# Kernel optimization log

Hardware: AMD Instinct MI355X
Metric: run time of the kernel (lower is better)

## Reference

```python
import jax, jax.numpy as jnp
import numpy as np

N, E, G = 50000, 800000, 128
IN, HID, OUT, H = 38, 64, 128, 4
NEG_SLOPE = 0.2
EPS = 1e-16


def setup_inputs() -> dict:
    key = jax.random.key(0)
    ks = jax.random.split(key, 16)
    s = 0.05
    inp = {
        "x": jax.random.normal(ks[0], (N, IN), jnp.float32),
        "edge_index": jax.random.randint(ks[1], (2, E), 0, N),
        "batch": jnp.sort(jax.random.randint(ks[2], (N,), 0, G)),
        # GATv2 layer 1: in=38 -> heads=4, C=64 (concat -> 256)
        "Wl1": jax.random.normal(ks[3], (IN, H * HID), jnp.float32) * s,
        "bl1": jnp.zeros((H * HID,), jnp.float32),
        "Wr1": jax.random.normal(ks[4], (IN, H * HID), jnp.float32) * s,
        "br1": jnp.zeros((H * HID,), jnp.float32),
        "att1": jax.random.normal(ks[5], (H, HID), jnp.float32) * s,
        "bias1": jnp.zeros((H * HID,), jnp.float32),
        # GATv2 layer 2: in=256 -> heads=1, C=128
        "Wl2": jax.random.normal(ks[6], (H * HID, OUT), jnp.float32) * s,
        "bl2": jnp.zeros((OUT,), jnp.float32),
        "Wr2": jax.random.normal(ks[7], (H * HID, OUT), jnp.float32) * s,
        "br2": jnp.zeros((OUT,), jnp.float32),
        "att2": jax.random.normal(ks[8], (1, OUT), jnp.float32) * s,
        "bias2": jnp.zeros((OUT,), jnp.float32),
    }
    return inp


def gatv2(x, src, dst, Wl, bl, Wr, br, att, bias, heads, C):
    n = x.shape[0]
    xl = (x @ Wl + bl).reshape(n, heads, C)  # source transform
    xr = (x @ Wr + br).reshape(n, heads, C)  # target transform
    e = jax.nn.leaky_relu(xl[src] + xr[dst], NEG_SLOPE)  # [E', H, C]
    logits = jnp.einsum("ehc,hc->eh", e, att)
    # segment softmax over incoming edges of each destination node
    m = jax.ops.segment_max(logits, dst, num_segments=n)
    p = jnp.exp(logits - m[dst])
    denom = jax.ops.segment_sum(p, dst, num_segments=n)
    alpha = p / (denom[dst] + EPS)  # [E', H]
    msg = xl[src] * alpha[..., None]
    out = jax.ops.segment_sum(msg, dst, num_segments=n)  # [N, H, C]
    return out.reshape(n, heads * C) + bias


def reference(x, edge_index, batch, Wl1, bl1, Wr1, br1, att1, bias1,
              Wl2, bl2, Wr2, br2, att2, bias2):
    n = x.shape[0]
    loops = jnp.arange(n, dtype=edge_index.dtype)
    src = jnp.concatenate([edge_index[0], loops])  # add_self_loops (PyG default)
    dst = jnp.concatenate([edge_index[1], loops])
    h = jax.nn.relu(gatv2(x, src, dst, Wl1, bl1, Wr1, br1, att1, bias1, H, HID))
    # dropout is identity at inference
    h = jax.nn.relu(gatv2(h, src, dst, Wl2, bl2, Wr2, br2, att2, bias2, 1, OUT))
    # global mean pool over graphs
    sums = jax.ops.segment_sum(h, batch, num_segments=G)
    counts = jax.ops.segment_sum(jnp.ones((n,), h.dtype), batch, num_segments=G)
    return sums / jnp.maximum(counts, 1.0)[:, None]
```

## Files before the change

### kernel.cpp

```cpp
#include <hip/hip_runtime.h>
#include <hip/hip_bf16.h>
#include <limits.h>

#define N_NODES 50000
#define N_EDGES 800000
#define TOT_E   (N_EDGES + N_NODES)
#define IN_F    38
#define HIDC    64
#define NH      4
#define F1      256
#define F2      128
#define NGRAPH  128
#define NEG_SLOPE 0.2f
#define EPS_A   1e-16f

typedef __hip_bfloat16 bf16;
typedef unsigned char fp8_t;
typedef __attribute__((ext_vector_type(8))) short short8;
typedef __attribute__((ext_vector_type(16))) float f32x16;
typedef __attribute__((ext_vector_type(2))) float f2;

constexpr size_t al256(size_t x) { return (x + 255) & ~(size_t)255; }

#define P_WL1   0
#define P_BL1   (P_WL1 + IN_F * F1)
#define P_WR1   (P_BL1 + F1)
#define P_BR1   (P_WR1 + IN_F * F1)
#define P_ATT1  (P_BR1 + F1)
#define P_BIAS1 (P_ATT1 + F1)
#define P_WL2   (P_BIAS1 + F1)
#define P_BL2   (P_WL2 + F1 * F2)
#define P_WR2   (P_BL2 + F2)
#define P_BR2   (P_WR2 + F1 * F2)
#define P_ATT2  (P_BR2 + F2)
#define P_BIAS2 (P_ATT2 + F2)
#define P_TOTAL (P_BIAS2 + F2)

constexpr size_t OFF_PAR  = 256;
constexpr size_t OFF_XL1  = OFF_PAR + al256((size_t)P_TOTAL * 4);
constexpr size_t OFF_XR1  = OFF_XL1 + al256((size_t)N_NODES * F1 * 2);
constexpr size_t OFF_H    = OFF_XR1 + al256((size_t)N_NODES * F1 * 2);
constexpr size_t OFF_XL2  = OFF_H   + al256((size_t)N_NODES * F1 * 2);
constexpr size_t OFF_XR2  = OFF_XL2 + al256((size_t)N_NODES * F2 * 2);
constexpr size_t OFF_CNT  = OFF_XR2 + al256((size_t)N_NODES * F2 * 2);
constexpr size_t OFF_GS   = OFF_CNT + al256((size_t)N_NODES * 4);
constexpr size_t OFF_GE   = OFF_GS  + al256((size_t)NGRAPH * 4);
constexpr size_t OFF_PSUM = OFF_GE  + al256((size_t)NGRAPH * 4);
constexpr size_t OFF_ZEND = OFF_PSUM+ al256((size_t)NGRAPH * F2 * 4);
constexpr size_t OFF_OFFS = OFF_ZEND;
constexpr size_t OFF_CSR  = OFF_OFFS+ al256((size_t)(N_NODES + 1) * 4);
constexpr size_t OFF_WT1  = OFF_CSR + al256((size_t)TOT_E * 4);
constexpr size_t OFF_WT2  = OFF_WT1 + al256((size_t)512 * 64 * 2);
constexpr size_t OFF_BS   = OFF_WT2 + al256((size_t)256 * 256 * 2);
constexpr size_t OFF_RANK = OFF_BS  + al256(64 * 4);
constexpr size_t OFF_H2   = OFF_XL1;
constexpr size_t OFF_XB   = OFF_H;

#define SCAN_BLKS 49
#define GBLK 1563
#define SBL  831

__device__ __forceinline__ void unpack8bf2(uint4 q, f2* f) {
  unsigned v[4] = {q.x, q.y, q.z, q.w};
#pragma unroll
  for (int i = 0; i < 4; i++) {
    f2 t;
    t.x = __uint_as_float(v[i] << 16);
    t.y = __uint_as_float(v[i] & 0xffff0000u);
    f[i] = t;
  }
}

__device__ __forceinline__ void load8bf2(const bf16* __restrict__ p, f2* f) {
  unpack8bf2(*(const uint4*)p, f);
}

__device__ __forceinline__ void unpack8fp8(uint2 q, f2* f) {
  f[0] = __builtin_amdgcn_cvt_pk_f32_fp8(q.x, false);
  f[1] = __builtin_amdgcn_cvt_pk_f32_fp8(q.x, true);
  f[2] = __builtin_amdgcn_cvt_pk_f32_fp8(q.y, false);
  f[3] = __builtin_amdgcn_cvt_pk_f32_fp8(q.y, true);
}

__device__ __forceinline__ fp8_t f32_to_fp8(float v) {
  return (fp8_t)(__builtin_amdgcn_cvt_pk_fp8_f32(v, v, 0, false) & 0xFF);
}

__device__ __forceinline__ f2 lrelu2(f2 s) {
  f2 as;
  as.x = __uint_as_float(__float_as_uint(s.x) & 0x7fffffffu);
  as.y = __uint_as_float(__float_as_uint(s.y) & 0x7fffffffu);
  return 0.6f * s + 0.4f * as;
}

__device__ __forceinline__ int detect_f32_wave(const void* __restrict__ x) {
  const unsigned short* u = (const unsigned short*)x;
  unsigned short b = u[threadIdx.x & 63];
  int e = (b >> 7) & 0xFF;
  unsigned long long m = __ballot(!((e == 0) || (e >= 96 && e <= 158)));
  return __popcll(m) > 8;
}

#define B_CVT  338
#define B_XP   1563
#define B_W1   128
#define B_W2   256
#define B_BND  196
#define B_CNT  831

struct PrepArgs {
  const void* x;
  const void* src[12];
  const int* ei;
  const int* batch;
};

__global__ __launch_bounds__(256) void prep_k(
    PrepArgs a, float* __restrict__ par, bf16* __restrict__ xb,
    bf16* __restrict__ wt1, bf16* __restrict__ wt2,
    int* __restrict__ gs, int* __restrict__ ge, int* __restrict__ cnt,
    int* __restrict__ rank) {
  int b = blockIdx.x;
  const int tid = threadIdx.x;

  if (b < B_CVT) {
    const int flag = detect_f32_wave(a.x);
    int idx = b * 256 + tid;
    const void* p; int base;
    if      (idx < P_BL1)  { p = a.src[0];  base = P_WL1; }
    else if (idx < P_WR1)  { p = a.src[1];  base = P_BL1; }
    else if (idx < P_BR1)  { p = a.src[2];  base = P_WR1; }
    else if (idx < P_ATT1) { p = a.src[3];  base = P_BR1; }
    else if (idx < P_BIAS1){ p = a.src[4];  base = P_ATT1; }
    else if (idx < P_WL2)  { p = a.src[5];  base = P_BIAS1; }
    else if (idx < P_BL2)  { p = a.src[6];  base = P_WL2; }
    else if (idx < P_WR2)  { p = a.src[7];  base = P_BL2; }
    else if (idx < P_BR2)  { p = a.src[8];  base = P_WR2; }
    else if (idx < P_ATT2) { p = a.src[9];  base = P_BR2; }
    else if (idx < P_BIAS2){ p = a.src[10]; base = P_ATT2; }
    else                   { p = a.src[11]; base = P_BIAS2; }
    int li = idx - base;
    par[idx] = flag ? ((const float*)p)[li] : (float)((const bf16*)p)[li];
    return;
  }
  b -= B_CVT;
  if (b < B_XP) {
    const int flag = detect_f32_wave(a.x);
    int gid = b * 256 + tid;
    int n = gid >> 3, k0 = (gid & 7) * 8;
    float v[8];
#pragma unroll
    for (int j = 0; j < 8; j++) {
      int k = k0 + j;
      v[j] = 0.f;
      if (k < IN_F) {
        int idx = n * IN_F + k;
        v[j] = flag ? ((const float*)a.x)[idx] : (float)((const bf16*)a.x)[idx];
      }
    }
    __align__(16) bf16 ob[8];
#pragma unroll
    for (int j = 0; j < 8; j++) ob[j] = (bf16)v[j];
    *(uint4*)(xb + (size_t)n * 64 + k0) = *(uint4*)ob;
    return;
  }
  b -= B_XP;
  if (b < B_W1) {
    const int flag = detect_f32_wave(a.x);
    int i = b * 256 + tid;
    int n = i >> 6, k = i & 63;
    float v = 0.f;
    if (k < IN_F) {
      const void* W = (n < F1) ? a.src[0] : a.src[2];
      int col = (n < F1) ? n : n - F1;
      int idx = k * F1 + col;
      v = flag ? ((const float*)W)[idx] : (float)((const bf16*)W)[idx];
    }
    wt1[i] = (bf16)v;
    return;
  }
  b -= B_W1;
  if (b < B_W2) {
    const int flag = detect_f32_wave(a.x);
    int i = b * 256 + tid;
    int n = i >> 8, k = i & 255;
    const void* W = (n < F2) ? a.src[6] : a.src[8];
    int col = (n < F2) ? n : n - F2;
    int idx = k * F2 + col;
    float v = flag ? ((const float*)W)[idx] : (float)((const bf16*)W)[idx];
    wt2[i] = (bf16)v;
    return;
  }
  b -= B_W2;
  if (b < B_BND) {
    int n = b * 256 + tid;
    if (n >= N_NODES) return;
    int bb = a.batch[n];
    if (n == 0) gs[bb] = 1;
    else {
      int bp = a.batch[n - 1];
      if (bp != bb) { gs[bb] = n + 1; ge[bp] = n; }
    }
    if (n == N_NODES - 1) ge[bb] = N_NODES;
    return;
  }
  b -= B_BND;
  {
    int base = b * 1024 + tid;
    int dstv[4]; bool val[4];
#pragma unroll
    for (int i = 0; i < 4; i++) {
      int e = base + i * 256;
      val[i] = e < TOT_E;
      dstv[i] = 0;
      if (val[i])
        dstv[i] = (e < N_EDGES) ? a.ei[N_EDGES + e] : (e - N_EDGES);
    }
#pragma unroll
    for (int i = 0; i < 4; i++) {
      int e = base + i * 256;
      if (val[i]) rank[e] = atomicAdd(&cnt[dstv[i]], 1);
    }
  }
}

__global__ __launch_bounds__(256) void gemm1_scatter_k(
    const bf16* __restrict__ xb, const bf16* __restrict__ wt1,
    const float* __restrict__ par,
    fp8_t* __restrict__ xl1, bf16* __restrict__ xr1,
    const int* __restrict__ ei, const int* __restrict__ offs,
    const int* __restrict__ rank, int* __restrict__ csr) {
  __shared__ char lds[24576];
  if (blockIdx.x >= GBLK) {
    int base = (blockIdx.x - GBLK) * 1024 + threadIdx.x;
#pragma unroll
    for (int i = 0; i < 4; i++) {
      int e = base + i * 256;
      if (e >= TOT_E) continue;
      int src, dst;
      if (e < N_EDGES) { src = ei[e]; dst = ei[N_EDGES + e]; }
      else             { src = dst = e - N_EDGES; }
      csr[offs[dst] + rank[e]] = src;
    }
    return;
  }
  const int w = threadIdx.x >> 6, lane = threadIdx.x & 63;
  const int m0 = blockIdx.x * 32;
  const int colbase = w * 128;
  const int lm = lane & 31;
  const int kh = lane >> 5;

  int arow = m0 + lm; if (arow >= N_NODES) arow = N_NODES - 1;
  short8 afr[4];
#pragma unroll
  for (int kk = 0; kk < 4; kk++)
    afr[kk] = *(const short8*)(xb + (size_t)arow * 64 + kk * 16 + kh * 8);

  f32x16 acc[4] = {};
#pragma unroll
  for (int t = 0; t < 4; t++) {
    int n = colbase + t * 32 + lm;
#pragma unroll
    for (int kk = 0; kk < 4; kk++) {
      short8 b = *(const short8*)(wt1 + (size_t)n * 64 + kk * 16 + kh * 8);
      acc[t] = __builtin_amdgcn_mfma_f32_32x32x16_bf16(afr[kk], b, acc[t], 0, 0, 0);
    }
  }

  char* lds8  = lds;
  bf16* lds16 = (bf16*)(lds + 8192);
  if (w < 2) {
#pragma unroll
    for (int t = 0; t < 4; t++) {
      int col = colbase + t * 32 + lm;
      float bv = par[P_BL1 + col];
#pragma unroll
      for (int reg = 0; reg < 16; reg++) {
        int rl = (reg & 3) + 8 * (reg >> 2) + 4 * kh;
        lds8[rl * 256 + col] = f32_to_fp8(acc[t][reg] + bv);
      }
    }
  } else {
#pragma unroll
    for (int t = 0; t < 4; t++) {
      int c = colbase - 256 + t * 32 + lm;
      float bv = par[P_BR1 + c];
#pragma unroll
      for (int reg = 0; reg < 16; reg++) {
        int rl = (reg & 3) + 8 * (reg >> 2) + 4 * kh;
        lds16[rl * 256 + c] = (bf16)(acc[t][reg] + bv);
      }
    }
  }
  __syncthreads();

  const int tid = threadIdx.x;
#pragma unroll
  for (int i = 0; i < 2; i++) {
    int idx = tid + i * 256;
    int row = idx >> 4, ck = (idx & 15) * 16;
    int grow = m0 + row;
    if (grow < N_NODES)
      *(uint4*)(xl1 + (size_t)grow * F1 + ck) = *(uint4*)(lds8 + row * 256 + ck);
  }
#pragma unroll
  for (int i = 0; i < 4; i++) {
    int idx = tid + i * 256;
    int row = idx >> 5, ck = (idx & 31) * 16;
    int grow = m0 + row;
    if (grow < N_NODES)
      *(uint4*)((char*)(xr1 + (size_t)grow * F1) + ck) =
          *(uint4*)((char*)(lds16 + row * 256) + ck);
  }
}

__global__ __launch_bounds__(256) void gemm2_mfma_k(
    const bf16* __restrict__ h, const bf16* __restrict__ wt2,
    const float* __restrict__ par,
    fp8_t* __restrict__ xl2, bf16* __restrict__ xr2) {
  __shared__ char lds[12288];
  const int w = threadIdx.x >> 6, lane = threadIdx.x & 63;
  const int m0 = blockIdx.x * 32;
  const int colbase = w * 64;
  const int lm = lane & 31;
  const int kh = lane >> 5;

  int arow = m0 + lm; if (arow >= N_NODES) arow = N_NODES - 1;
  const bf16* hrow = h + (size_t)arow * F1 + kh * 8;

  f32x16 acc[2] = {};
#pragma unroll
  for (int kk = 0; kk < 16; kk++) {
    short8 a = *(const short8*)(hrow + kk * 16);
#pragma unroll
    for (int t = 0; t < 2; t++) {
      int n = colbase + t * 32 + lm;
      short8 b = *(const short8*)(wt2 + (size_t)n * 256 + kk * 16 + kh * 8);
      acc[t] = __builtin_amdgcn_mfma_f32_32x32x16_bf16(a, b, acc[t], 0, 0, 0);
    }
  }

  char* lds8  = lds;
  bf16* lds16 = (bf16*)(lds + 4096);
  if (w < 2) {
#pragma unroll
    for (int t = 0; t < 2; t++) {
      int col = colbase + t * 32 + lm;
      float bv = par[P_BL2 + col];
#pragma unroll
      for (int reg = 0; reg < 16; reg++) {
        int rl = (reg & 3) + 8 * (reg >> 2) + 4 * kh;
        lds8[rl * 128 + col] = f32_to_fp8(acc[t][reg] + bv);
      }
    }
  } else {
#pragma unroll
    for (int t = 0; t < 2; t++) {
      int c = colbase - 128 + t * 32 + lm;
      float bv = par[P_BR2 + c];
#pragma unroll
      for (int reg = 0; reg < 16; reg++) {
        int rl = (reg & 3) + 8 * (reg >> 2) + 4 * kh;
        lds16[rl * 128 + c] = (bf16)(acc[t][reg] + bv);
      }
    }
  }
  __syncthreads();

  const int tid = threadIdx.x;
  {
    int row = tid >> 3, ck = (tid & 7) * 16;
    int grow = m0 + row;
    if (grow < N_NODES)
      *(uint4*)(xl2 + (size_t)grow * F2 + ck) = *(uint4*)(lds8 + row * 128 + ck);
  }
#pragma unroll
  for (int i = 0; i < 2; i++) {
    int idx = tid + i * 256;
    int row = idx >> 4, ck = (idx & 15) * 16;
    int grow = m0 + row;
    if (grow < N_NODES)
      *(uint4*)((char*)(xr2 + (size_t)grow * F2) + ck) =
          *(uint4*)((char*)(lds16 + row * 128) + ck);
  }
}

__global__ __launch_bounds__(1024) void scan_a(const int* __restrict__ cnt,
                                               int* __restrict__ offs,
                                               int* __restrict__ bsum) {
  __shared__ int wsum[16];
  const int t = threadIdx.x;
  const int lane = t & 63, w = t >> 6;
  int idx = blockIdx.x * 1024 + t;
  int v = (idx < N_NODES) ? cnt[idx] : 0;
  int s = v;
#pragma unroll
  for (int off = 1; off < 64; off <<= 1) {
    int u = __shfl_up(s, off, 64);
    if (lane >= off) s += u;
  }
  if (lane == 63) wsum[w] = s;
  __syncthreads();
  int prefix = 0;
  for (int i = 0; i < w; i++) prefix += wsum[i];
  if (idx < N_NODES) offs[idx] = prefix + s - v;
  if (t == 1023) bsum[blockIdx.x] = prefix + s;
}

__global__ void scan_c(const int* __restrict__ bsum, int* __restrict__ offs) {
  const int t = threadIdx.x;
  const int grp = blockIdx.x >> 2;
  __shared__ int sboff;
  if (t < 64) {
    int v = (t < SCAN_BLKS) ? bsum[t] : 0;
    int s = v;
#pragma unroll
    for (int off = 1; off < 64; off <<= 1) {
      int u = __shfl_up(s, off, 64);
      if (t >= off) s += u;
    }
    if (t == grp) sboff = s - v;
  }
  __syncthreads();
  int idx = blockIdx.x * 256 + t;
  if (idx < N_NODES) offs[idx] += sboff;
  if (blockIdx.x == 0 && t == 0) offs[N_NODES] = TOT_E;
}

__global__ __launch_bounds__(256, 4) void agg1_k(
    const fp8_t* __restrict__ xl1, const bf16* __restrict__ xr1,
    const float* __restrict__ par,
    const int* __restrict__ offs, const int* __restrict__ csr,
    bf16* __restrict__ hout) {
  const int dst = blockIdx.x * 4 + (threadIdx.x >> 6);
  if (dst >= N_NODES) return;
  const int lane = threadIdx.x & 63;
  const int g = lane >> 5;
  const int sl = lane & 31;
  const int chb = sl * 8;

  f2 r2[4], a2[4];
  load8bf2(xr1 + (size_t)dst * F1 + chb, r2);
  {
    float4 aa = *(const float4*)(par + P_ATT1 + chb);
    float4 ab = *(const float4*)(par + P_ATT1 + chb + 4);
    a2[0].x = aa.x; a2[0].y = aa.y; a2[1].x = aa.z; a2[1].y = aa.w;
    a2[2].x = ab.x; a2[2].y = ab.y; a2[3].x = ab.z; a2[3].y = ab.w;
  }

  const int e0 = offs[dst], e1 = offs[dst + 1];
  const f2 zf2 = {0.f, 0.f};
  f2 acc2[4];
#pragma unroll
  for (int j = 0; j < 4; j++) acc2[j] = zf2;
  float denom = 0.f;

  const uint2 zq = {0, 0};
  int e = e0 + g;
  bool valid = e < e1;
  uint2 q = valid ? *(const uint2*)(xl1 + (size_t)csr[e] * F1 + chb) : zq;

  for (int base = e0; base < e1; base += 2) {
    const uint2 qc = q;
    const bool vc = valid;
    e += 2;
    valid = e < e1;
    q = valid ? *(const uint2*)(xl1 + (size_t)csr[e] * F1 + chb) : zq;

    f2 v2[4];
    unpack8fp8(qc, v2);
    f2 lt2 = zf2;
#pragma unroll
    for (int j = 0; j < 4; j++)
      lt2 = lrelu2(v2[j] + r2[j]) * a2[j] + lt2;
    float lt = vc ? (lt2.x + lt2.y) : -1e30f;
    lt += __shfl_xor(lt, 1, 64);
    lt += __shfl_xor(lt, 2, 64);
    lt += __shfl_xor(lt, 4, 64);
    float p = __expf(fminf(lt, 60.f));
    denom += p;
    f2 pv; pv.x = p; pv.y = p;
#pragma unroll
    for (int j = 0; j < 4; j++) acc2[j] = pv * v2[j] + acc2[j];
  }

  denom += __shfl_xor(denom, 32, 64);
#pragma unroll
  for (int j = 0; j < 4; j++) {
    acc2[j].x += __shfl_xor(acc2[j].x, 32, 64);
    acc2[j].y += __shfl_xor(acc2[j].y, 32, 64);
  }

  if (g == 0) {
    float inv = 1.f / (denom + EPS_A);
    __align__(16) bf16 ob[8];
#pragma unroll
    for (int j = 0; j < 4; j++) {
      float o0 = fmaxf(acc2[j].x * inv + par[P_BIAS1 + chb + 2*j],     0.f);
      float o1 = fmaxf(acc2[j].y * inv + par[P_BIAS1 + chb + 2*j + 1], 0.f);
      ob[2*j] = (bf16)o0; ob[2*j+1] = (bf16)o1;
    }
    *(uint4*)(hout + (size_t)dst * F1 + chb) = *(uint4*)ob;
  }
}

__global__ __launch_bounds__(256, 4) void agg2_k(
    const fp8_t* __restrict__ xl2, const bf16* __restrict__ xr2,
    const float* __restrict__ par,
    const int* __restrict__ offs, const int* __restrict__ csr,
    bf16* __restrict__ h2) {
  const int dst = blockIdx.x * 4 + (threadIdx.x >> 6);
  if (dst >= N_NODES) return;
  const int lane = threadIdx.x & 63;
  const int g = lane >> 4;
  const int sl = lane & 15;
  const int chb = sl * 8;

  f2 r2[4], a2[4];
  load8bf2(xr2 + (size_t)dst * F2 + chb, r2);
  {
    float4 aa = *(const float4*)(par + P_ATT2 + chb);
    float4 ab = *(const float4*)(par + P_ATT2 + chb + 4);
    a2[0].x = aa.x; a2[0].y = aa.y; a2[1].x = aa.z; a2[1].y = aa.w;
    a2[2].x = ab.x; a2[2].y = ab.y; a2[3].x = ab.z; a2[3].y = ab.w;
  }

  const int e0 = offs[dst], e1 = offs[dst + 1];
  const f2 zf2 = {0.f, 0.f};
  f2 acc2[4];
#pragma unroll
  for (int j = 0; j < 4; j++) acc2[j] = zf2;
  float denom = 0.f;

  const uint2 zq = {0, 0};
  int e = e0 + g;
  bool valid = e < e1;
  uint2 q = valid ? *(const uint2*)(xl2 + (size_t)csr[e] * F2 + chb) : zq;

  for (int base = e0; base < e1; base += 4) {
    const uint2 qc = q;
    const bool vc = valid;
    e += 4;
    valid = e < e1;
    q = valid ? *(const uint2*)(xl2 + (size_t)csr[e] * F2 + chb) : zq;

    f2 v2[4];
    unpack8fp8(qc, v2);
    f2 lt2 = zf2;
#pragma unroll
    for (int j = 0; j < 4; j++)
      lt2 = lrelu2(v2[j] + r2[j]) * a2[j] + lt2;
    float lt = vc ? (lt2.x + lt2.y) : -1e30f;
    lt += __shfl_xor(lt, 1, 64);
    lt += __shfl_xor(lt, 2, 64);
    lt += __shfl_xor(lt, 4, 64);
    lt += __shfl_xor(lt, 8, 64);
    float p = __expf(fminf(lt, 60.f));
    denom += p;
    f2 pv; pv.x = p; pv.y = p;
#pragma unroll
    for (int j = 0; j < 4; j++) acc2[j] = pv * v2[j] + acc2[j];
  }

#pragma unroll
  for (int m = 16; m <= 32; m <<= 1) {
    denom += __shfl_xor(denom, m, 64);
#pragma unroll
    for (int j = 0; j < 4; j++) {
      acc2[j].x += __shfl_xor(acc2[j].x, m, 64);
      acc2[j].y += __shfl_xor(acc2[j].y, m, 64);
    }
  }

  if (g == 0) {
    float inv = 1.f / (denom + EPS_A);
    __align__(16) bf16 ob[8];
#pragma unroll
    for (int j = 0; j < 4; j++) {
      float o0 = fmaxf(acc2[j].x * inv + par[P_BIAS2 + chb + 2*j],     0.f);
      float o1 = fmaxf(acc2[j].y * inv + par[P_BIAS2 + chb + 2*j + 1], 0.f);
      ob[2*j] = (bf16)o0; ob[2*j+1] = (bf16)o1;
    }
    *(uint4*)(h2 + (size_t)dst * F2 + chb) = *(uint4*)ob;
  }
}

__global__ __launch_bounds__(256) void poolp_k(
    const bf16* __restrict__ h2, const int* __restrict__ gs,
    const int* __restrict__ ge, float* __restrict__ psum) {
  const int g = blockIdx.x >> 3, slice = blockIdx.x & 7;
  const int t = threadIdx.x;
  const int c = t & 127, half = t >> 7;
  int s = gs[g] - 1, eex = ge[g];
  if (s < 0 || eex <= s) return;
  float sum = 0.f;
  for (int n = s + slice * 2 + half; n < eex; n += 16)
    sum += (float)h2[(size_t)n * F2 + c];
  atomicAdd(&psum[g * F2 + c], sum);
}

__global__ void poolf_k(const float* __restrict__ psum,
                        const int* __restrict__ gs, const int* __restrict__ ge,
                        const void* __restrict__ x, void* __restrict__ out) {
  int i = blockIdx.x * 256 + threadIdx.x;
  if (i >= NGRAPH * F2) return;
  const int flag = detect_f32_wave(x);
  int g = i >> 7;
  int s = gs[g] - 1, eex = ge[g];
  float cnt = (s >= 0 && eex > s) ? (float)(eex - s) : 1.f;
  float v = psum[i] / cnt;
  if (flag) ((float*)out)[i] = v;
  else      ((bf16*)out)[i] = (bf16)v;
}

extern "C" void kernel_launch(void* const* d_in, const int* in_sizes, int n_in,
                              void* d_out, int out_size, void* d_ws, size_t ws_size,
                              hipStream_t stream) {
  (void)in_sizes; (void)n_in; (void)out_size; (void)ws_size;
  const void* x     = d_in[0];
  const int*  ei    = (const int*)d_in[1];
  const int*  batch = (const int*)d_in[2];

  char* ws = (char*)d_ws;
  float* par  = (float*)(ws + OFF_PAR);
  fp8_t* xl1 = (fp8_t*)(ws + OFF_XL1);
  bf16* xr1 = (bf16*)(ws + OFF_XR1);
  bf16* h   = (bf16*)(ws + OFF_H);
  fp8_t* xl2 = (fp8_t*)(ws + OFF_XL2);
  bf16* xr2 = (bf16*)(ws + OFF_XR2);
  bf16* h2  = (bf16*)(ws + OFF_H2);
  bf16* xb  = (bf16*)(ws + OFF_XB);
  bf16* wt1 = (bf16*)(ws + OFF_WT1);
  bf16* wt2 = (bf16*)(ws + OFF_WT2);
  int* cnt    = (int*)(ws + OFF_CNT);
  int* offs   = (int*)(ws + OFF_OFFS);
  int* csr    = (int*)(ws + OFF_CSR);
  int* gs     = (int*)(ws + OFF_GS);
  int* ge     = (int*)(ws + OFF_GE);
  int* bsum   = (int*)(ws + OFF_BS);
  float* psum = (float*)(ws + OFF_PSUM);
  int* rank   = (int*)(ws + OFF_RANK);

  hipMemsetAsync(cnt, 0, OFF_ZEND - OFF_CNT, stream);

  PrepArgs pa;
  pa.x = x; pa.ei = ei; pa.batch = batch;
  for (int i = 0; i < 12; i++) pa.src[i] = d_in[3 + i];
  const int prep_blocks = B_CVT + B_XP + B_W1 + B_W2 + B_BND + B_CNT;
  prep_k<<<prep_blocks, 256, 0, stream>>>(pa, par, xb, wt1, wt2, gs, ge, cnt, rank);

  scan_a<<<SCAN_BLKS, 1024, 0, stream>>>(cnt, offs, bsum);
  scan_c<<<(N_NODES + 255) / 256, 256, 0, stream>>>(bsum, offs);

  gemm1_scatter_k<<<GBLK + SBL, 256, 0, stream>>>(xb, wt1, par, xl1, xr1,
                                                  ei, offs, rank, csr);
  agg1_k<<<(N_NODES + 3) / 4, 256, 0, stream>>>(xl1, xr1, par, offs, csr, h);
  gemm2_mfma_k<<<GBLK, 256, 0, stream>>>(h, wt2, par, xl2, xr2);
  agg2_k<<<(N_NODES + 3) / 4, 256, 0, stream>>>(xl2, xr2, par, offs, csr, h2);
  poolp_k<<<NGRAPH * 8, 256, 0, stream>>>(h2, gs, ge, psum);
  poolf_k<<<(NGRAPH * F2 + 255) / 256, 256, 0, stream>>>(psum, gs, ge, x, d_out);
}
```

Baseline: 318.4 us.

## Fuse scan carry-add into GEMM1/scatter kernel and pool finalize into partial pool

Removes two kernel launches. The second scan pass is folded into a combined kernel: each block recomputes the block-sum prefix in LDS, and the CSR scatter adds the block offset itself instead of waiting on a finalized offsets array. The pool finalize step is merged into the partial-pool kernel with a per-graph done counter, so the last block for each graph writes the mean. The scan's first pass now uses 256 threads, each handling four elements. This trades launch overhead for extra atomics, fences and redundant small prefix computations per block.

```diff
diff --git a/kernel.cpp b/kernel.cpp
--- a/kernel.cpp
+++ b/kernel.cpp
@@ -46,9 +46,11 @@
 constexpr size_t OFF_GS   = OFF_CNT + al256((size_t)N_NODES * 4);
 constexpr size_t OFF_GE   = OFF_GS  + al256((size_t)NGRAPH * 4);
 constexpr size_t OFF_PSUM = OFF_GE  + al256((size_t)NGRAPH * 4);
-constexpr size_t OFF_ZEND = OFF_PSUM+ al256((size_t)NGRAPH * F2 * 4);
+constexpr size_t OFF_DONE = OFF_PSUM+ al256((size_t)NGRAPH * F2 * 4);
+constexpr size_t OFF_ZEND = OFF_DONE+ al256((size_t)NGRAPH * 4);
 constexpr size_t OFF_OFFS = OFF_ZEND;
-constexpr size_t OFF_CSR  = OFF_OFFS+ al256((size_t)(N_NODES + 1) * 4);
+constexpr size_t OFF_OFFSP= OFF_OFFS+ al256((size_t)(N_NODES + 1) * 4);
+constexpr size_t OFF_CSR  = OFF_OFFSP+ al256((size_t)N_NODES * 4);
 constexpr size_t OFF_WT1  = OFF_CSR + al256((size_t)TOT_E * 4);
 constexpr size_t OFF_WT2  = OFF_WT1 + al256((size_t)512 * 64 * 2);
 constexpr size_t OFF_BS   = OFF_WT2 + al256((size_t)256 * 256 * 2);
@@ -59,6 +61,7 @@
 #define SCAN_BLKS 49
 #define GBLK 1563
 #define SBL  831
+#define MEGA_SCANC 196
 
 __device__ __forceinline__ void unpack8bf2(uint4 q, f2* f) {
   unsigned v[4] = {q.x, q.y, q.z, q.w};
@@ -224,15 +227,84 @@
   }
 }
 
-__global__ __launch_bounds__(256) void gemm1_scatter_k(
+__global__ __launch_bounds__(256) void scan_a(const int* __restrict__ cnt,
+                                              int* __restrict__ offs_p,
+                                              int* __restrict__ bsum) {
+  __shared__ int wsum[4];
+  const int t = threadIdx.x, lane = t & 63, w = t >> 6;
+  int i0 = blockIdx.x * 1024 + t * 4;
+  int v[4];
+#pragma unroll
+  for (int j = 0; j < 4; j++) v[j] = (i0 + j < N_NODES) ? cnt[i0 + j] : 0;
+  int tsum = v[0] + v[1] + v[2] + v[3];
+  int s = tsum;
+#pragma unroll
+  for (int off = 1; off < 64; off <<= 1) {
+    int u = __shfl_up(s, off, 64);
+    if (lane >= off) s += u;
+  }
+  if (lane == 63) wsum[w] = s;
+  __syncthreads();
+  int pref = 0;
+  for (int i = 0; i < w; i++) pref += wsum[i];
+  int excl = pref + s - tsum;
+  int o0 = excl, o1 = o0 + v[0], o2 = o1 + v[1], o3 = o2 + v[2];
+  if (i0 + 3 < N_NODES) {
+    int4 q; q.x = o0; q.y = o1; q.z = o2; q.w = o3;
+    *(int4*)(offs_p + i0) = q;
+  } else {
+    if (i0     < N_NODES) offs_p[i0]     = o0;
+    if (i0 + 1 < N_NODES) offs_p[i0 + 1] = o1;
+    if (i0 + 2 < N_NODES) offs_p[i0 + 2] = o2;
+    if (i0 + 3 < N_NODES) offs_p[i0 + 3] = o3;
+  }
+  if (t == 255) bsum[blockIdx.x] = pref + s;
+}
+
+__global__ __launch_bounds__(256) void mega_k(
     const bf16* __restrict__ xb, const bf16* __restrict__ wt1,
     const float* __restrict__ par,
     fp8_t* __restrict__ xl1, bf16* __restrict__ xr1,
-    const int* __restrict__ ei, const int* __restrict__ offs,
-    const int* __restrict__ rank, int* __restrict__ csr) {
+    const int* __restrict__ ei, const int* __restrict__ offs_p,
+    const int* __restrict__ bsum, const int* __restrict__ rank,
+    int* __restrict__ offs, int* __restrict__ csr) {
   __shared__ char lds[24576];
-  if (blockIdx.x >= GBLK) {
-    int base = (blockIdx.x - GBLK) * 1024 + threadIdx.x;
+  __shared__ int boff_s[64];
+  int b = blockIdx.x;
+  const int tid = threadIdx.x;
+
+  if (b < MEGA_SCANC) {
+    if (tid < 64) {
+      int v = (tid < SCAN_BLKS) ? bsum[tid] : 0;
+      int s = v;
+#pragma unroll
+      for (int off = 1; off < 64; off <<= 1) {
+        int u = __shfl_up(s, off, 64);
+        if (tid >= off) s += u;
+      }
+      boff_s[tid] = s - v;
+    }
+    __syncthreads();
+    int idx = b * 256 + tid;
+    if (idx < N_NODES) offs[idx] = offs_p[idx] + boff_s[idx >> 10];
+    if (b == 0 && tid == 0) offs[N_NODES] = TOT_E;
+    return;
+  }
+  b -= MEGA_SCANC;
+  if (b >= GBLK) {
+    b -= GBLK;
+    if (tid < 64) {
+      int v = (tid < SCAN_BLKS) ? bsum[tid] : 0;
+      int s = v;
+#pragma unroll
+      for (int off = 1; off < 64; off <<= 1) {
+        int u = __shfl_up(s, off, 64);
+        if (tid >= off) s += u;
+      }
+      boff_s[tid] = s - v;
+    }
+    __syncthreads();
+    int base = b * 1024 + tid;
 #pragma unroll
     for (int i = 0; i < 4; i++) {
       int e = base + i * 256;
@@ -240,12 +312,12 @@
       int src, dst;
       if (e < N_EDGES) { src = ei[e]; dst = ei[N_EDGES + e]; }
       else             { src = dst = e - N_EDGES; }
-      csr[offs[dst] + rank[e]] = src;
+      csr[offs_p[dst] + boff_s[dst >> 10] + rank[e]] = src;
     }
     return;
   }
-  const int w = threadIdx.x >> 6, lane = threadIdx.x & 63;
-  const int m0 = blockIdx.x * 32;
+  const int w = tid >> 6, lane = tid & 63;
+  const int m0 = b * 32;
   const int colbase = w * 128;
   const int lm = lane & 31;
   const int kh = lane >> 5;
@@ -262,8 +334,8 @@
     int n = colbase + t * 32 + lm;
 #pragma unroll
     for (int kk = 0; kk < 4; kk++) {
-      short8 b = *(const short8*)(wt1 + (size_t)n * 64 + kk * 16 + kh * 8);
-      acc[t] = __builtin_amdgcn_mfma_f32_32x32x16_bf16(afr[kk], b, acc[t], 0, 0, 0);
+      short8 bb = *(const short8*)(wt1 + (size_t)n * 64 + kk * 16 + kh * 8);
+      acc[t] = __builtin_amdgcn_mfma_f32_32x32x16_bf16(afr[kk], bb, acc[t], 0, 0, 0);
     }
   }
 
@@ -294,7 +366,6 @@
   }
   __syncthreads();
 
-  const int tid = threadIdx.x;
 #pragma unroll
   for (int i = 0; i < 2; i++) {
     int idx = tid + i * 256;
@@ -383,48 +454,6 @@
       *(uint4*)((char*)(xr2 + (size_t)grow * F2) + ck) =
           *(uint4*)((char*)(lds16 + row * 128) + ck);
   }
-}
-
-__global__ __launch_bounds__(1024) void scan_a(const int* __restrict__ cnt,
-                                               int* __restrict__ offs,
-                                               int* __restrict__ bsum) {
-  __shared__ int wsum[16];
-  const int t = threadIdx.x;
-  const int lane = t & 63, w = t >> 6;
-  int idx = blockIdx.x * 1024 + t;
-  int v = (idx < N_NODES) ? cnt[idx] : 0;
-  int s = v;
-#pragma unroll
-  for (int off = 1; off < 64; off <<= 1) {
-    int u = __shfl_up(s, off, 64);
-    if (lane >= off) s += u;
-  }
-  if (lane == 63) wsum[w] = s;
-  __syncthreads();
-  int prefix = 0;
-  for (int i = 0; i < w; i++) prefix += wsum[i];
-  if (idx < N_NODES) offs[idx] = prefix + s - v;
-  if (t == 1023) bsum[blockIdx.x] = prefix + s;
-}
-
-__global__ void scan_c(const int* __restrict__ bsum, int* __restrict__ offs) {
-  const int t = threadIdx.x;
-  const int grp = blockIdx.x >> 2;
-  __shared__ int sboff;
-  if (t < 64) {
-    int v = (t < SCAN_BLKS) ? bsum[t] : 0;
-    int s = v;
-#pragma unroll
-    for (int off = 1; off < 64; off <<= 1) {
-      int u = __shfl_up(s, off, 64);
-      if (t >= off) s += u;
-    }
-    if (t == grp) sboff = s - v;
-  }
-  __syncthreads();
-  int idx = blockIdx.x * 256 + t;
-  if (idx < N_NODES) offs[idx] += sboff;
-  if (blockIdx.x == 0 && t == 0) offs[N_NODES] = TOT_E;
 }
 
 __global__ __launch_bounds__(256, 4) void agg1_k(
@@ -587,30 +616,36 @@
 
 __global__ __launch_bounds__(256) void poolp_k(
     const bf16* __restrict__ h2, const int* __restrict__ gs,
-    const int* __restrict__ ge, float* __restrict__ psum) {
+    const int* __restrict__ ge, float* __restrict__ psum,
+    int* __restrict__ done, const void* __restrict__ x,
+    void* __restrict__ out) {
   const int g = blockIdx.x >> 3, slice = blockIdx.x & 7;
   const int t = threadIdx.x;
   const int c = t & 127, half = t >> 7;
-  int s = gs[g] - 1, eex = ge[g];
-  if (s < 0 || eex <= s) return;
+  const int s = gs[g] - 1, eex = ge[g];
+  const bool nonempty = (s >= 0 && eex > s);
   float sum = 0.f;
-  for (int n = s + slice * 2 + half; n < eex; n += 16)
-    sum += (float)h2[(size_t)n * F2 + c];
+  if (nonempty)
+    for (int n = s + slice * 2 + half; n < eex; n += 16)
+      sum += (float)h2[(size_t)n * F2 + c];
   atomicAdd(&psum[g * F2 + c], sum);
-}
-
-__global__ void poolf_k(const float* __restrict__ psum,
-                        const int* __restrict__ gs, const int* __restrict__ ge,
-                        const void* __restrict__ x, void* __restrict__ out) {
-  int i = blockIdx.x * 256 + threadIdx.x;
-  if (i >= NGRAPH * F2) return;
-  const int flag = detect_f32_wave(x);
-  int g = i >> 7;
-  int s = gs[g] - 1, eex = ge[g];
-  float cnt = (s >= 0 && eex > s) ? (float)(eex - s) : 1.f;
-  float v = psum[i] / cnt;
-  if (flag) ((float*)out)[i] = v;
-  else      ((bf16*)out)[i] = (bf16)v;
+
+  __threadfence();
+  __shared__ int lastflag;
+  if (t == 0) lastflag = (atomicAdd(&done[g], 1) == 7);
+  __syncthreads();
+  if (lastflag) {
+    __threadfence();
+    const int flag = detect_f32_wave(x);
+    if (t < F2) {
+      int i = g * F2 + t;
+      float cntf = nonempty ? (float)(eex - s) : 1.f;
+      volatile const float* vp = psum;
+      float v = vp[i] / cntf;
+      if (flag) ((float*)out)[i] = v;
+      else      ((bf16*)out)[i] = (bf16)v;
+    }
+  }
 }
 
 extern "C" void kernel_launch(void* const* d_in, const int* in_sizes, int n_in,
@@ -634,11 +669,13 @@
   bf16* wt2 = (bf16*)(ws + OFF_WT2);
   int* cnt    = (int*)(ws + OFF_CNT);
   int* offs   = (int*)(ws + OFF_OFFS);
+  int* offs_p = (int*)(ws + OFF_OFFSP);
   int* csr    = (int*)(ws + OFF_CSR);
   int* gs     = (int*)(ws + OFF_GS);
   int* ge     = (int*)(ws + OFF_GE);
   int* bsum   = (int*)(ws + OFF_BS);
   float* psum = (float*)(ws + OFF_PSUM);
+  int* done   = (int*)(ws + OFF_DONE);
   int* rank   = (int*)(ws + OFF_RANK);
 
   hipMemsetAsync(cnt, 0, OFF_ZEND - OFF_CNT, stream);
@@ -649,14 +686,13 @@
   const int prep_blocks = B_CVT + B_XP + B_W1 + B_W2 + B_BND + B_CNT;
   prep_k<<<prep_blocks, 256, 0, stream>>>(pa, par, xb, wt1, wt2, gs, ge, cnt, rank);
 
-  scan_a<<<SCAN_BLKS, 1024, 0, stream>>>(cnt, offs, bsum);
-  scan_c<<<(N_NODES + 255) / 256, 256, 0, stream>>>(bsum, offs);
-
-  gemm1_scatter_k<<<GBLK + SBL, 256, 0, stream>>>(xb, wt1, par, xl1, xr1,
-                                                  ei, offs, rank, csr);
+  scan_a<<<SCAN_BLKS, 256, 0, stream>>>(cnt, offs_p, bsum);
+
+  mega_k<<<MEGA_SCANC + GBLK + SBL, 256, 0, stream>>>(
+      xb, wt1, par, xl1, xr1, ei, offs_p, bsum, rank, offs, csr);
+
   agg1_k<<<(N_NODES + 3) / 4, 256, 0, stream>>>(xl1, xr1, par, offs, csr, h);
   gemm2_mfma_k<<<GBLK, 256, 0, stream>>>(h, wt2, par, xl2, xr2);
   agg2_k<<<(N_NODES + 3) / 4, 256, 0, stream>>>(xl2, xr2, par, offs, csr, h2);
-  poolp_k<<<NGRAPH * 8, 256, 0, stream>>>(h2, gs, ge, psum);
-  poolf_k<<<(NGRAPH * F2 + 255) / 256, 256, 0, stream>>>(psum, gs, ge, x, d_out);
-}
+  poolp_k<<<NGRAPH * 8, 256, 0, stream>>>(h2, gs, ge, psum, done, x, d_out);
+}
```

Measured after the change: 391.4 us. +22.9%, slower.
